# Kernel optimization log

Hardware: AMD Instinct MI355X
Metric: run time of the kernel (lower is better)

## Reference

```python
import jax, jax.numpy as jnp
import numpy as np
from jax import lax

INP_MODES = (4, 8, 8, 4)
OUT_MODES = (4, 8, 8, 4)
RANKS = (1, 8, 8, 8, 1)  # mat_ranks
WINDOW = (3, 3)


def setup_inputs() -> dict:
    key = jax.random.key(0)
    ks = jax.random.split(key, 7)
    d = {}
    d["x"] = jax.random.normal(ks[0], (16, 32, 32, 1024), jnp.float32)
    # conv filter: [kh, kw, 1, r0]
    d["filters"] = jax.random.normal(ks[1], (WINDOW[0], WINDOW[1], 1, RANKS[0]), jnp.float32) * (1.0 / 3.0)
    # TT cores: core_i has shape [m_i * r_{i+1}, r_i * n_i]
    for i in range(4):
        shp = (OUT_MODES[i] * RANKS[i + 1], RANKS[i] * INP_MODES[i])
        d[f"core{i}"] = jax.random.normal(ks[2 + i], shp, jnp.float32) * (1.0 / np.sqrt(shp[1]).astype(np.float32))
    d["bias"] = jnp.zeros((int(np.prod(OUT_MODES)),), jnp.float32)
    return d


def tt_conv(x, filters, cores, bias):
    B, H, W, C = x.shape  # C == prod(INP_MODES)
    r0 = filters.shape[3]
    # depthwise-style: every channel of every batch item becomes its own 1-channel map
    tmp = x.transpose(0, 3, 1, 2).reshape(B * C, H, W, 1)
    tmp = lax.conv_general_dilated(tmp, filters, window_strides=(1, 1), padding="SAME",
                                   dimension_numbers=("NHWC", "HWIO", "NHWC"))
    h, w = tmp.shape[1], tmp.shape[2]
    # [B, C, h, w, r0] -> [r0, C, B, h, w]
    tmp = tmp.reshape(B, C, h, w, r0).transpose(4, 1, 0, 2, 3)
    # chained TT-core contractions (fixed small loop over num_dim)
    for i in range(len(cores)):
        tmp = tmp.reshape(RANKS[i] * INP_MODES[i], -1)
        tmp = cores[i] @ tmp                      # [m_i * r_{i+1}, rest]
        tmp = tmp.reshape(OUT_MODES[i], -1).T     # move m_i to the back
    M = int(np.prod(OUT_MODES))
    out = tmp.reshape(-1, h, w, M) + bias
    return jax.nn.relu(out)


def reference(x, filters, core0, core1, core2, core3, bias):
    return tt_conv(x, filters, [core0, core1, core2, core3], bias)
```

## Files before the change

### kernel.cpp

```cpp
#include <hip/hip_runtime.h>
#include <hip/hip_bf16.h>
#include <stdint.h>

typedef __attribute__((ext_vector_type(8))) short short8;
typedef __attribute__((ext_vector_type(4))) float f32x4;

__device__ inline unsigned short f2bf(float f) {
  union { float f; unsigned u; } v; v.f = f;
  unsigned r = v.u + 0x7fffu + ((v.u >> 16) & 1u);
  return (unsigned short)(r >> 16);
}

__global__ __launch_bounds__(256) void tt_build_T(
    const float* __restrict__ c0, const float* __restrict__ c1,
    const float* __restrict__ c2, const float* __restrict__ c3,
    unsigned short* __restrict__ Tb) {
  __shared__ float L[8192];
  __shared__ float R[8192];
  int t = threadIdx.x;
  for (int i = t; i < 8192; i += 256) {
    int n1 = i & 7, n0 = (i >> 3) & 3, r2 = (i >> 5) & 7, m1 = (i >> 8) & 7, m0 = i >> 11;
    float s = 0.f;
#pragma unroll
    for (int r1 = 0; r1 < 8; ++r1)
      s += c0[(m0 * 8 + r1) * 4 + n0] * c1[(m1 * 8 + r2) * 64 + r1 * 8 + n1];
    L[i] = s;
  }
  for (int i = t; i < 8192; i += 256) {
    int n3 = i & 3, n2 = (i >> 2) & 7, m3 = (i >> 5) & 3, m2 = (i >> 7) & 7, r2 = i >> 10;
    float s = 0.f;
#pragma unroll
    for (int r3 = 0; r3 < 8; ++r3)
      s += c2[(m2 * 8 + r3) * 64 + r2 * 8 + n2] * c3[m3 * 32 + r3 * 4 + n3];
    R[i] = s;
  }
  __syncthreads();
  int base = blockIdx.x * 4096;
  for (int j = 0; j < 16; ++j) {
    int lin = j * 256 + t;
    int g = base + lin;
    int m = g >> 10, n = g & 1023;
    int m0 = m >> 8, m1 = (m >> 5) & 7, m2 = (m >> 2) & 7, m3 = m & 3;
    int n0 = n >> 8, n1 = (n >> 5) & 7, n2 = (n >> 2) & 7, n3 = n & 3;
    float s = 0.f;
#pragma unroll
    for (int r2 = 0; r2 < 8; ++r2)
      s += L[(((m0 * 8 + m1) * 8 + r2) * 4 + n0) * 8 + n1] *
           R[(((r2 * 8 + m2) * 4 + m3) * 8 + n2) * 4 + n3];
    Tb[(size_t)m * 1024 + n] = f2bf(s);
  }
}

__global__ __launch_bounds__(256) void tt_conv3x3_lds(
    const float* __restrict__ x, const float* __restrict__ filt,
    unsigned short* __restrict__ D) {
  __shared__ float xs[10][32][32];
  int bid = blockIdx.x;
  int cg = bid & 31, strip = (bid >> 5) & 3, b = bid >> 7;
  int h0 = strip * 8;
  int tid = threadIdx.x;
  float4 z4; z4.x = z4.y = z4.z = z4.w = 0.f;
#pragma unroll
  for (int i = 0; i < 10; ++i) {
    int j = tid + 256 * i;
    int row = j >> 8, w = (j >> 3) & 31, c4 = j & 7;
    int gh = h0 - 1 + row;
    float4 v = z4;
    if ((unsigned)gh < 32u)
      v = *reinterpret_cast<const float4*>(x + ((size_t)((b * 32 + gh) * 32 + w)) * 1024 + cg * 32 + c4 * 4);
    *reinterpret_cast<float4*>(&xs[row][w][c4 * 4]) = v;
  }
  float F[9];
#pragma unroll
  for (int i = 0; i < 9; ++i) F[i] = filt[i];
  __syncthreads();

  int c4 = tid & 7, w = tid >> 3;
#define LD3(r, d0, d1, d2) { \
    d1 = *reinterpret_cast<const float4*>(&xs[r][w][c4 * 4]); \
    d0 = (w > 0)  ? *reinterpret_cast<const float4*>(&xs[r][w - 1][c4 * 4]) : z4; \
    d2 = (w < 31) ? *reinterpret_cast<const float4*>(&xs[r][w + 1][c4 * 4]) : z4; }
#define ACC4(a, f, v) { a.x += (f) * v.x; a.y += (f) * v.y; a.z += (f) * v.z; a.w += (f) * v.w; }
  float4 a00, a01, a02, a10, a11, a12, a20, a21, a22;
  LD3(0, a00, a01, a02);
  LD3(1, a10, a11, a12);
#pragma unroll
  for (int h = 0; h < 8; ++h) {
    LD3(h + 2, a20, a21, a22);
    float4 s = z4;
    ACC4(s, F[0], a00); ACC4(s, F[1], a01); ACC4(s, F[2], a02);
    ACC4(s, F[3], a10); ACC4(s, F[4], a11); ACC4(s, F[5], a12);
    ACC4(s, F[6], a20); ACC4(s, F[7], a21); ACC4(s, F[8], a22);
    ushort4 o;
    o.x = f2bf(s.x); o.y = f2bf(s.y); o.z = f2bf(s.z); o.w = f2bf(s.w);
    *reinterpret_cast<ushort4*>(&D[((size_t)(b * 1024 + (h0 + h) * 32 + w)) * 1024 + cg * 32 + c4 * 4]) = o;
    a00 = a10; a01 = a11; a02 = a12;
    a10 = a20; a11 = a21; a12 = a22;
  }
#undef LD3
#undef ACC4
}

__device__ inline void stage16(const unsigned short* g, unsigned short* l) {
  __builtin_amdgcn_global_load_lds(
      (const __attribute__((address_space(1))) void*)g,
      (__attribute__((address_space(3))) void*)l, 16, 0, 0);
}

__global__ __launch_bounds__(512, 2) void tt_gemm_w1(
    const unsigned short* __restrict__ A,
    const unsigned short* __restrict__ Bt,
    const float* __restrict__ bias,
    float* __restrict__ C) {
  __shared__ unsigned short lds[3][2][8192];
  const int tid = threadIdx.x;
  const int lane = tid & 63, wave = tid >> 6;
  const int wr = wave >> 2, wc = wave & 3;
  const int lr = lane & 15, kc = lane >> 4;

  int lin = blockIdx.x + blockIdx.y * 64;
  int Lg = ((lin & 7) << 5) | (lin >> 3);
  int brow = (Lg & 63) * 256;
  int bcol = (Lg >> 6) * 256;

  int rowq0, cq0, rowq1, cq1;
  { int q = tid;       int li = q >> 3, sp = q & 7, sl = sp ^ (li & 7); rowq0 = 2 * li + (sl >> 2); cq0 = sl & 3; }
  { int q = tid + 512; int li = q >> 3, sp = q & 7, sl = sp ^ (li & 7); rowq1 = 2 * li + (sl >> 2); cq1 = sl & 3; }
  const unsigned short* srcA0 = A + (size_t)(brow + rowq0) * 1024 + cq0 * 8;
  const unsigned short* srcA1 = A + (size_t)(brow + rowq1) * 1024 + cq1 * 8;
  const unsigned short* srcB0 = Bt + (size_t)(bcol + rowq0) * 1024 + cq0 * 8;
  const unsigned short* srcB1 = Bt + (size_t)(bcol + rowq1) * 1024 + cq1 * 8;
  const int l0 = tid * 8, l1 = (tid + 512) * 8;

  int offA[8], offB[4];
#pragma unroll
  for (int m = 0; m < 8; ++m) {
    int row = wr * 128 + m * 16 + lr;
    int li = row >> 1, sl = (row & 1) * 4 + kc;
    offA[m] = (li * 8 + (sl ^ (li & 7))) * 8;
  }
#pragma unroll
  for (int n = 0; n < 4; ++n) {
    int row = wc * 64 + n * 16 + lr;
    int li = row >> 1, sl = (row & 1) * 4 + kc;
    offB[n] = (li * 8 + (sl ^ (li & 7))) * 8;
  }

  f32x4 acc[8][4] = {};

#define STAGE(S, T) { \
    stage16(srcA0 + (T) * 32, &lds[S][0][l0]); \
    stage16(srcA1 + (T) * 32, &lds[S][0][l1]); \
    stage16(srcB0 + (T) * 32, &lds[S][1][l0]); \
    stage16(srcB1 + (T) * 32, &lds[S][1][l1]); }

#define KTILE(RB, SB, T2, VMS) { \
    if ((T2) >= 0) STAGE(SB, T2); \
    asm volatile("s_waitcnt vmcnt(" VMS ")" ::: "memory"); \
    __builtin_amdgcn_s_barrier(); \
    short8 af[8], bfr[4]; \
    _Pragma("unroll") for (int m = 0; m < 8; ++m) \
      af[m] = *reinterpret_cast<const short8*>(&lds[RB][0][offA[m]]); \
    _Pragma("unroll") for (int n = 0; n < 4; ++n) \
      bfr[n] = *reinterpret_cast<const short8*>(&lds[RB][1][offB[n]]); \
    _Pragma("unroll") for (int m = 0; m < 8; ++m) \
      _Pragma("unroll") for (int n = 0; n < 4; ++n) \
        acc[m][n] = __builtin_amdgcn_mfma_f32_16x16x32_bf16(bfr[n], af[m], acc[m][n], 0, 0, 0); \
    __builtin_amdgcn_s_barrier(); \
    __builtin_amdgcn_sched_barrier(0); }

  STAGE(0, 0);
  STAGE(1, 1);

  for (int t = 0; t < 30; t += 3) {
    KTILE(0, 2, t + 2, "8")
    KTILE(1, 0, t + 3, "8")
    KTILE(2, 1, t + 4, "8")
  }
  KTILE(0, 0, -1, "4")
  KTILE(1, 1, -1, "0")

#undef KTILE
#undef STAGE

#pragma unroll
  for (int n = 0; n < 4; ++n) {
    int col = bcol + wc * 64 + n * 16 + kc * 4;
    float4 bv = *reinterpret_cast<const float4*>(&bias[col]);
#pragma unroll
    for (int m = 0; m < 8; ++m) {
      int row = brow + wr * 128 + m * 16 + lr;
      f32x4 v = acc[m][n];
      float4 o;
      o.x = v[0] + bv.x; o.y = v[1] + bv.y; o.z = v[2] + bv.z; o.w = v[3] + bv.w;
      o.x = o.x > 0.f ? o.x : 0.f;
      o.y = o.y > 0.f ? o.y : 0.f;
      o.z = o.z > 0.f ? o.z : 0.f;
      o.w = o.w > 0.f ? o.w : 0.f;
      *reinterpret_cast<float4*>(&C[(size_t)row * 1024 + col]) = o;
    }
  }
}

extern "C" void kernel_launch(void* const* d_in, const int* in_sizes, int n_in,
                              void* d_out, int out_size, void* d_ws, size_t ws_size,
                              hipStream_t stream) {
  const float* x = (const float*)d_in[0];
  const float* filt = (const float*)d_in[1];
  const float* c0 = (const float*)d_in[2];
  const float* c1 = (const float*)d_in[3];
  const float* c2 = (const float*)d_in[4];
  const float* c3 = (const float*)d_in[5];
  const float* bias = (const float*)d_in[6];
  float* out = (float*)d_out;

  unsigned short* Tb = (unsigned short*)d_ws;
  unsigned short* D = Tb + (size_t)1024 * 1024;

  tt_build_T<<<256, 256, 0, stream>>>(c0, c1, c2, c3, Tb);
  tt_conv3x3_lds<<<2048, 256, 0, stream>>>(x, filt, D);
  dim3 grid(64, 4);
  tt_gemm_w1<<<grid, 512, 0, stream>>>(D, Tb, bias, out);
}
```

Measured before the change: 80.68 us.

## Fuse 3x3 conv into GEMM mainloop, computing bf16 A tiles in LDS

```diff
diff --git a/kernel.cpp b/kernel.cpp
--- a/kernel.cpp
+++ b/kernel.cpp
@@ -3,6 +3,7 @@
 #include <stdint.h>
 
 typedef __attribute__((ext_vector_type(8))) short short8;
+typedef __attribute__((ext_vector_type(8))) unsigned short u16x8;
 typedef __attribute__((ext_vector_type(4))) float f32x4;
 
 __device__ inline unsigned short f2bf(float f) {
@@ -51,136 +52,154 @@
   }
 }
 
-__global__ __launch_bounds__(256) void tt_conv3x3_lds(
-    const float* __restrict__ x, const float* __restrict__ filt,
-    unsigned short* __restrict__ D) {
-  __shared__ float xs[10][32][32];
-  int bid = blockIdx.x;
-  int cg = bid & 31, strip = (bid >> 5) & 3, b = bid >> 7;
-  int h0 = strip * 8;
-  int tid = threadIdx.x;
-  float4 z4; z4.x = z4.y = z4.z = z4.w = 0.f;
-#pragma unroll
-  for (int i = 0; i < 10; ++i) {
-    int j = tid + 256 * i;
-    int row = j >> 8, w = (j >> 3) & 31, c4 = j & 7;
-    int gh = h0 - 1 + row;
-    float4 v = z4;
-    if ((unsigned)gh < 32u)
-      v = *reinterpret_cast<const float4*>(x + ((size_t)((b * 32 + gh) * 32 + w)) * 1024 + cg * 32 + c4 * 4);
-    *reinterpret_cast<float4*>(&xs[row][w][c4 * 4]) = v;
-  }
-  float F[9];
-#pragma unroll
-  for (int i = 0; i < 9; ++i) F[i] = filt[i];
-  __syncthreads();
-
-  int c4 = tid & 7, w = tid >> 3;
-#define LD3(r, d0, d1, d2) { \
-    d1 = *reinterpret_cast<const float4*>(&xs[r][w][c4 * 4]); \
-    d0 = (w > 0)  ? *reinterpret_cast<const float4*>(&xs[r][w - 1][c4 * 4]) : z4; \
-    d2 = (w < 31) ? *reinterpret_cast<const float4*>(&xs[r][w + 1][c4 * 4]) : z4; }
-#define ACC4(a, f, v) { a.x += (f) * v.x; a.y += (f) * v.y; a.z += (f) * v.z; a.w += (f) * v.w; }
-  float4 a00, a01, a02, a10, a11, a12, a20, a21, a22;
-  LD3(0, a00, a01, a02);
-  LD3(1, a10, a11, a12);
-#pragma unroll
-  for (int h = 0; h < 8; ++h) {
-    LD3(h + 2, a20, a21, a22);
-    float4 s = z4;
-    ACC4(s, F[0], a00); ACC4(s, F[1], a01); ACC4(s, F[2], a02);
-    ACC4(s, F[3], a10); ACC4(s, F[4], a11); ACC4(s, F[5], a12);
-    ACC4(s, F[6], a20); ACC4(s, F[7], a21); ACC4(s, F[8], a22);
-    ushort4 o;
-    o.x = f2bf(s.x); o.y = f2bf(s.y); o.z = f2bf(s.z); o.w = f2bf(s.w);
-    *reinterpret_cast<ushort4*>(&D[((size_t)(b * 1024 + (h0 + h) * 32 + w)) * 1024 + cg * 32 + c4 * 4]) = o;
-    a00 = a10; a01 = a11; a02 = a12;
-    a10 = a20; a11 = a21; a12 = a22;
-  }
-#undef LD3
-#undef ACC4
-}
-
-__device__ inline void stage16(const unsigned short* g, unsigned short* l) {
+__device__ inline void stage16(const void* g, void* l) {
   __builtin_amdgcn_global_load_lds(
       (const __attribute__((address_space(1))) void*)g,
       (__attribute__((address_space(3))) void*)l, 16, 0, 0);
 }
 
-__global__ __launch_bounds__(512, 2) void tt_gemm_w1(
-    const unsigned short* __restrict__ A,
-    const unsigned short* __restrict__ Bt,
-    const float* __restrict__ bias,
-    float* __restrict__ C) {
-  __shared__ unsigned short lds[3][2][8192];
+#define XB0 0
+#define XB1 40960
+#define AB  81920
+#define BB0 98304
+#define BB1 114688
+
+__global__ __launch_bounds__(512, 2) void tt_fused(
+    const float* __restrict__ x, const float* __restrict__ filt,
+    const unsigned short* __restrict__ Bt, const float* __restrict__ bias,
+    const float* __restrict__ zp, float* __restrict__ C) {
+  __shared__ __align__(16) char lds[131072];
   const int tid = threadIdx.x;
   const int lane = tid & 63, wave = tid >> 6;
   const int wr = wave >> 2, wc = wave & 3;
   const int lr = lane & 15, kc = lane >> 4;
 
-  int lin = blockIdx.x + blockIdx.y * 64;
-  int Lg = ((lin & 7) << 5) | (lin >> 3);
-  int brow = (Lg & 63) * 256;
-  int bcol = (Lg >> 6) * 256;
-
-  int rowq0, cq0, rowq1, cq1;
-  { int q = tid;       int li = q >> 3, sp = q & 7, sl = sp ^ (li & 7); rowq0 = 2 * li + (sl >> 2); cq0 = sl & 3; }
-  { int q = tid + 512; int li = q >> 3, sp = q & 7, sl = sp ^ (li & 7); rowq1 = 2 * li + (sl >> 2); cq1 = sl & 3; }
-  const unsigned short* srcA0 = A + (size_t)(brow + rowq0) * 1024 + cq0 * 8;
-  const unsigned short* srcA1 = A + (size_t)(brow + rowq1) * 1024 + cq1 * 8;
-  const unsigned short* srcB0 = Bt + (size_t)(bcol + rowq0) * 1024 + cq0 * 8;
-  const unsigned short* srcB1 = Bt + (size_t)(bcol + rowq1) * 1024 + cq1 * 8;
-  const int l0 = tid * 8, l1 = (tid + 512) * 8;
+  int bid = blockIdx.x;
+  int lin = (bid & 7) * 32 + (bid >> 3);
+  int np = lin >> 6, mt = lin & 63;
+  int b = mt >> 2, h0 = (mt & 3) * 8;
+  int brow = mt * 256, bcol = np * 256;
+
+  const float* xsrc[5];
+  int xstep[5], xdst[5];
+#pragma unroll
+  for (int i = 0; i < 5; ++i) {
+    int q = tid + 512 * i;
+    int r = q >> 8, w = (q >> 3) & 31;
+    int c4 = (q & 7) ^ ((w & 3) << 1);
+    int gh = h0 - 1 + r;
+    bool ok = (unsigned)gh < 32u;
+    xsrc[i] = ok ? x + (((size_t)(b * 32 + gh) * 32 + w) << 10) + c4 * 4
+                 : zp + ((q & 2047) << 2);
+    xstep[i] = ok ? 32 : 0;
+    xdst[i] = q * 16;
+  }
+  const unsigned short* bsrc[2];
+  int bdst[2];
+#pragma unroll
+  for (int j = 0; j < 2; ++j) {
+    int q = tid + 512 * j;
+    int li = q >> 3, sl = (q & 7) ^ (li & 7);
+    int row = 2 * li + (sl >> 2), ck = sl & 3;
+    bsrc[j] = Bt + (size_t)(bcol + row) * 1024 + ck * 8;
+    bdst[j] = q * 16;
+  }
+
+  const int cg = tid & 3, cw = (tid >> 2) & 31, hp = tid >> 7;
+  const int lr0 = 2 * hp;
+  int wo0, wo1;
+  {
+    int pp = lr0 * 32 + cw;
+    int li = pp >> 1, sl = (pp & 1) * 4 + cg;
+    wo0 = AB + li * 128 + (sl ^ (li & 7)) * 16;
+    pp += 32;
+    li = pp >> 1; sl = (pp & 1) * 4 + cg;
+    wo1 = AB + li * 128 + (sl ^ (li & 7)) * 16;
+  }
+  float F[9];
+#pragma unroll
+  for (int i = 0; i < 9; ++i) F[i] = filt[i];
 
   int offA[8], offB[4];
 #pragma unroll
   for (int m = 0; m < 8; ++m) {
     int row = wr * 128 + m * 16 + lr;
     int li = row >> 1, sl = (row & 1) * 4 + kc;
-    offA[m] = (li * 8 + (sl ^ (li & 7))) * 8;
+    offA[m] = AB + li * 128 + (sl ^ (li & 7)) * 16;
   }
 #pragma unroll
   for (int n = 0; n < 4; ++n) {
     int row = wc * 64 + n * 16 + lr;
     int li = row >> 1, sl = (row & 1) * 4 + kc;
-    offB[n] = (li * 8 + (sl ^ (li & 7))) * 8;
+    offB[n] = li * 128 + (sl ^ (li & 7)) * 16;
   }
 
   f32x4 acc[8][4] = {};
-
-#define STAGE(S, T) { \
-    stage16(srcA0 + (T) * 32, &lds[S][0][l0]); \
-    stage16(srcA1 + (T) * 32, &lds[S][0][l1]); \
-    stage16(srcB0 + (T) * 32, &lds[S][1][l0]); \
-    stage16(srcB1 + (T) * 32, &lds[S][1][l1]); }
-
-#define KTILE(RB, SB, T2, VMS) { \
-    if ((T2) >= 0) STAGE(SB, T2); \
-    asm volatile("s_waitcnt vmcnt(" VMS ")" ::: "memory"); \
-    __builtin_amdgcn_s_barrier(); \
+  const float4 z4 = {0.f, 0.f, 0.f, 0.f};
+
+#define STAGE(XOFF, BOFF, T) { \
+    _Pragma("unroll") for (int i = 0; i < 5; ++i) \
+      stage16(xsrc[i] + (size_t)(T) * xstep[i], lds + (XOFF) + xdst[i]); \
+    _Pragma("unroll") for (int j = 0; j < 2; ++j) \
+      stage16(bsrc[j] + (T) * 32, lds + (BOFF) + bdst[j]); }
+
+#define CONV(XOFF) { \
+    float4 s0a = z4, s0b = z4, s1a = z4, s1b = z4; \
+    _Pragma("unroll") for (int rr = 0; rr < 4; ++rr) { \
+      _Pragma("unroll") for (int dw = 0; dw < 3; ++dw) { \
+        int wq = cw + dw - 1; \
+        float4 va = z4, vb = z4; \
+        if ((unsigned)wq < 32u) { \
+          const char* p = lds + (XOFF) + (lr0 + rr) * 4096 + wq * 128 + \
+                          (((2 * cg) ^ ((wq & 3) << 1)) * 16); \
+          va = *reinterpret_cast<const float4*>(p); \
+          vb = *reinterpret_cast<const float4*>(p + 16); \
+        } \
+        if (rr < 3) { float f = F[rr * 3 + dw]; \
+          s0a.x += f * va.x; s0a.y += f * va.y; s0a.z += f * va.z; s0a.w += f * va.w; \
+          s0b.x += f * vb.x; s0b.y += f * vb.y; s0b.z += f * vb.z; s0b.w += f * vb.w; } \
+        if (rr > 0) { float f = F[(rr - 1) * 3 + dw]; \
+          s1a.x += f * va.x; s1a.y += f * va.y; s1a.z += f * va.z; s1a.w += f * va.w; \
+          s1b.x += f * vb.x; s1b.y += f * vb.y; s1b.z += f * vb.z; s1b.w += f * vb.w; } \
+      } \
+    } \
+    u16x8 o; \
+    o[0] = f2bf(s0a.x); o[1] = f2bf(s0a.y); o[2] = f2bf(s0a.z); o[3] = f2bf(s0a.w); \
+    o[4] = f2bf(s0b.x); o[5] = f2bf(s0b.y); o[6] = f2bf(s0b.z); o[7] = f2bf(s0b.w); \
+    *reinterpret_cast<u16x8*>(lds + wo0) = o; \
+    o[0] = f2bf(s1a.x); o[1] = f2bf(s1a.y); o[2] = f2bf(s1a.z); o[3] = f2bf(s1a.w); \
+    o[4] = f2bf(s1b.x); o[5] = f2bf(s1b.y); o[6] = f2bf(s1b.z); o[7] = f2bf(s1b.w); \
+    *reinterpret_cast<u16x8*>(lds + wo1) = o; }
+
+#define MFMA_PH(BOFF) { \
     short8 af[8], bfr[4]; \
     _Pragma("unroll") for (int m = 0; m < 8; ++m) \
-      af[m] = *reinterpret_cast<const short8*>(&lds[RB][0][offA[m]]); \
+      af[m] = *reinterpret_cast<const short8*>(lds + offA[m]); \
     _Pragma("unroll") for (int n = 0; n < 4; ++n) \
-      bfr[n] = *reinterpret_cast<const short8*>(&lds[RB][1][offB[n]]); \
+      bfr[n] = *reinterpret_cast<const short8*>(lds + (BOFF) + offB[n]); \
     _Pragma("unroll") for (int m = 0; m < 8; ++m) \
       _Pragma("unroll") for (int n = 0; n < 4; ++n) \
-        acc[m][n] = __builtin_amdgcn_mfma_f32_16x16x32_bf16(bfr[n], af[m], acc[m][n], 0, 0, 0); \
+        acc[m][n] = __builtin_amdgcn_mfma_f32_16x16x32_bf16(bfr[n], af[m], acc[m][n], 0, 0, 0); }
+
+#define TILE(T, XR, BR, XS, BS) { \
+    asm volatile("s_waitcnt vmcnt(0)" ::: "memory"); \
     __builtin_amdgcn_s_barrier(); \
-    __builtin_amdgcn_sched_barrier(0); }
-
-  STAGE(0, 0);
-  STAGE(1, 1);
-
-  for (int t = 0; t < 30; t += 3) {
-    KTILE(0, 2, t + 2, "8")
-    KTILE(1, 0, t + 3, "8")
-    KTILE(2, 1, t + 4, "8")
-  }
-  KTILE(0, 0, -1, "4")
-  KTILE(1, 1, -1, "0")
-
-#undef KTILE
+    asm volatile("" ::: "memory"); \
+    if ((T) + 1 < 32) STAGE(XS, BS, (T) + 1); \
+    CONV(XR); \
+    asm volatile("s_waitcnt lgkmcnt(0)" ::: "memory"); \
+    __builtin_amdgcn_s_barrier(); \
+    MFMA_PH(BR); }
+
+  STAGE(XB0, BB0, 0);
+  for (int t = 0; t < 32; t += 2) {
+    TILE(t, XB0, BB0, XB1, BB1)
+    TILE(t + 1, XB1, BB1, XB0, BB0)
+  }
+
+#undef TILE
+#undef MFMA_PH
+#undef CONV
 #undef STAGE
 
 #pragma unroll
@@ -215,10 +234,9 @@
   float* out = (float*)d_out;
 
   unsigned short* Tb = (unsigned short*)d_ws;
-  unsigned short* D = Tb + (size_t)1024 * 1024;
-
+  float* zp = (float*)((char*)d_ws + (2u << 20));
+
+  hipMemsetAsync(zp, 0, 65536, stream);
   tt_build_T<<<256, 256, 0, stream>>>(c0, c1, c2, c3, Tb);
-  tt_conv3x3_lds<<<2048, 256, 0, stream>>>(x, filt, D);
-  dim3 grid(64, 4);
-  tt_gemm_w1<<<grid, 512, 0, stream>>>(D, Tb, bias, out);
-}
+  tt_fused<<<256, 512, 0, stream>>>(x, filt, Tb, bias, zp, out);
+}
```

Result: slower. 221.1 us (+174.0%).

## Restructure GEMM mainloop into eight-phase pipeline with split A/B staging and setprio

Applied to the files above, without the earlier changes.

```diff
diff --git a/kernel.cpp b/kernel.cpp
--- a/kernel.cpp
+++ b/kernel.cpp
@@ -107,12 +107,13 @@
       (__attribute__((address_space(3))) void*)l, 16, 0, 0);
 }
 
-__global__ __launch_bounds__(512, 2) void tt_gemm_w1(
+__global__ __launch_bounds__(512, 2) void tt_gemm_8t(
     const unsigned short* __restrict__ A,
     const unsigned short* __restrict__ Bt,
     const float* __restrict__ bias,
     float* __restrict__ C) {
-  __shared__ unsigned short lds[3][2][8192];
+  __shared__ __align__(16) unsigned short Ah[2][2][8192];
+  __shared__ __align__(16) unsigned short Bh[2][2][8192];
   const int tid = threadIdx.x;
   const int lane = tid & 63, wave = tid >> 6;
   const int wr = wave >> 2, wc = wave & 3;
@@ -123,14 +124,14 @@
   int brow = (Lg & 63) * 256;
   int bcol = (Lg >> 6) * 256;
 
-  int rowq0, cq0, rowq1, cq1;
-  { int q = tid;       int li = q >> 3, sp = q & 7, sl = sp ^ (li & 7); rowq0 = 2 * li + (sl >> 2); cq0 = sl & 3; }
-  { int q = tid + 512; int li = q >> 3, sp = q & 7, sl = sp ^ (li & 7); rowq1 = 2 * li + (sl >> 2); cq1 = sl & 3; }
-  const unsigned short* srcA0 = A + (size_t)(brow + rowq0) * 1024 + cq0 * 8;
-  const unsigned short* srcA1 = A + (size_t)(brow + rowq1) * 1024 + cq1 * 8;
-  const unsigned short* srcB0 = Bt + (size_t)(bcol + rowq0) * 1024 + cq0 * 8;
-  const unsigned short* srcB1 = Bt + (size_t)(bcol + rowq1) * 1024 + cq1 * 8;
-  const int l0 = tid * 8, l1 = (tid + 512) * 8;
+  int row0, k0, row1, k1;
+  { int q = tid;       int li = q >> 3, c = (q & 7) ^ (li & 7); row0 = 2 * li + (c >> 2); k0 = (c & 3) * 8; }
+  { int q = tid + 512; int li = q >> 3, c = (q & 7) ^ (li & 7); row1 = 2 * li + (c >> 2); k1 = (c & 3) * 8; }
+  const unsigned short* pa0 = A + (size_t)(brow + row0) * 1024 + k0;
+  const unsigned short* pa1 = A + (size_t)(brow + row1) * 1024 + k1;
+  const unsigned short* pb0 = Bt + (size_t)(bcol + row0) * 1024 + k0;
+  const unsigned short* pb1 = Bt + (size_t)(bcol + row1) * 1024 + k1;
+  const int la0 = tid * 8, la1 = (tid + 512) * 8;
 
   int offA[8], offB[4];
 #pragma unroll
@@ -147,41 +148,71 @@
   }
 
   f32x4 acc[8][4] = {};
-
-#define STAGE(S, T) { \
-    stage16(srcA0 + (T) * 32, &lds[S][0][l0]); \
-    stage16(srcA1 + (T) * 32, &lds[S][0][l1]); \
-    stage16(srcB0 + (T) * 32, &lds[S][1][l0]); \
-    stage16(srcB1 + (T) * 32, &lds[S][1][l1]); }
-
-#define KTILE(RB, SB, T2, VMS) { \
-    if ((T2) >= 0) STAGE(SB, T2); \
-    asm volatile("s_waitcnt vmcnt(" VMS ")" ::: "memory"); \
+  short8 bfr[4];
+
+#define ST_A(D, KH, KT) do { \
+    stage16(pa0 + (KT) * 64 + (KH) * 32, &Ah[D][KH][la0]); \
+    stage16(pa1 + (KT) * 64 + (KH) * 32, &Ah[D][KH][la1]); } while (0)
+#define ST_B(D, KH, KT) do { \
+    stage16(pb0 + (KT) * 64 + (KH) * 32, &Bh[D][KH][la0]); \
+    stage16(pb1 + (KT) * 64 + (KH) * 32, &Bh[D][KH][la1]); } while (0)
+#define VM8 asm volatile("s_waitcnt vmcnt(8)" ::: "memory")
+#define VM4 asm volatile("s_waitcnt vmcnt(4)" ::: "memory")
+#define VM0 asm volatile("s_waitcnt vmcnt(0)" ::: "memory")
+#define NOPV (void)0
+
+#define PH(D, KK, MH, LOADB, STG, TV) { \
+    if (LOADB) { \
+      _Pragma("unroll") for (int n = 0; n < 4; ++n) \
+        bfr[n] = *reinterpret_cast<const short8*>(&Bh[D][KK][offB[n]]); \
+    } \
+    short8 af[4]; \
+    _Pragma("unroll") for (int m = 0; m < 4; ++m) \
+      af[m] = *reinterpret_cast<const short8*>(&Ah[D][KK][offA[(MH) * 4 + m]]); \
+    STG; \
     __builtin_amdgcn_s_barrier(); \
-    short8 af[8], bfr[4]; \
-    _Pragma("unroll") for (int m = 0; m < 8; ++m) \
-      af[m] = *reinterpret_cast<const short8*>(&lds[RB][0][offA[m]]); \
-    _Pragma("unroll") for (int n = 0; n < 4; ++n) \
-      bfr[n] = *reinterpret_cast<const short8*>(&lds[RB][1][offB[n]]); \
-    _Pragma("unroll") for (int m = 0; m < 8; ++m) \
+    asm volatile("s_waitcnt lgkmcnt(0)" ::: "memory"); \
+    __builtin_amdgcn_s_setprio(1); \
+    _Pragma("unroll") for (int m = 0; m < 4; ++m) \
       _Pragma("unroll") for (int n = 0; n < 4; ++n) \
-        acc[m][n] = __builtin_amdgcn_mfma_f32_16x16x32_bf16(bfr[n], af[m], acc[m][n], 0, 0, 0); \
-    __builtin_amdgcn_s_barrier(); \
-    __builtin_amdgcn_sched_barrier(0); }
-
-  STAGE(0, 0);
-  STAGE(1, 1);
-
-  for (int t = 0; t < 30; t += 3) {
-    KTILE(0, 2, t + 2, "8")
-    KTILE(1, 0, t + 3, "8")
-    KTILE(2, 1, t + 4, "8")
-  }
-  KTILE(0, 0, -1, "4")
-  KTILE(1, 1, -1, "0")
-
-#undef KTILE
-#undef STAGE
+        acc[(MH) * 4 + m][n] = __builtin_amdgcn_mfma_f32_16x16x32_bf16(bfr[n], af[m], acc[(MH) * 4 + m][n], 0, 0, 0); \
+    __builtin_amdgcn_s_setprio(0); \
+    TV; \
+    __builtin_amdgcn_s_barrier(); }
+
+  ST_A(0, 0, 0); ST_B(0, 0, 0);
+  ST_A(0, 1, 0); ST_B(0, 1, 0);
+  ST_A(1, 0, 1); ST_B(1, 0, 1);
+  VM8;
+  __builtin_amdgcn_s_barrier();
+
+  for (int i = 0; i < 7; ++i) {
+    int t = 2 * i;
+    PH(0, 0, 0, 1, ST_A(1, 1, t + 1), NOPV)
+    PH(0, 0, 1, 0, ST_B(1, 1, t + 1), VM8)
+    PH(0, 1, 0, 1, ST_A(0, 0, t + 2), NOPV)
+    PH(0, 1, 1, 0, ST_B(0, 0, t + 2), VM8)
+    PH(1, 0, 0, 1, ST_A(0, 1, t + 2), NOPV)
+    PH(1, 0, 1, 0, ST_B(0, 1, t + 2), VM8)
+    PH(1, 1, 0, 1, ST_A(1, 0, t + 3), NOPV)
+    PH(1, 1, 1, 0, ST_B(1, 0, t + 3), VM8)
+  }
+  PH(0, 0, 0, 1, ST_A(1, 1, 15), NOPV)
+  PH(0, 0, 1, 0, ST_B(1, 1, 15), VM8)
+  PH(0, 1, 0, 1, NOPV, NOPV)
+  PH(0, 1, 1, 0, NOPV, VM4)
+  PH(1, 0, 0, 1, NOPV, NOPV)
+  PH(1, 0, 1, 0, NOPV, VM0)
+  PH(1, 1, 0, 1, NOPV, NOPV)
+  PH(1, 1, 1, 0, NOPV, NOPV)
+
+#undef PH
+#undef ST_A
+#undef ST_B
+#undef VM8
+#undef VM4
+#undef VM0
+#undef NOPV
 
 #pragma unroll
   for (int n = 0; n < 4; ++n) {
@@ -220,5 +251,5 @@
   tt_build_T<<<256, 256, 0, stream>>>(c0, c1, c2, c3, Tb);
   tt_conv3x3_lds<<<2048, 256, 0, stream>>>(x, filt, D);
   dim3 grid(64, 4);
-  tt_gemm_w1<<<grid, 512, 0, stream>>>(D, Tb, bias, out);
-}
+  tt_gemm_8t<<<grid, 512, 0, stream>>>(D, Tb, bias, out);
+}
```

After: 85.38 us. +5.8%, slower.

## Merge prep kernels and register-double-buffer GEMM with 4-stage LDS ring

Applied to the files above, without the earlier changes.

```diff
diff --git a/kernel.cpp b/kernel.cpp
--- a/kernel.cpp
+++ b/kernel.cpp
@@ -10,55 +10,59 @@
   unsigned r = v.u + 0x7fffu + ((v.u >> 16) & 1u);
   return (unsigned short)(r >> 16);
 }
-
-__global__ __launch_bounds__(256) void tt_build_T(
+__device__ inline float bf2f(unsigned short u) {
+  union { unsigned u; float f; } v; v.u = ((unsigned)u) << 16; return v.f;
+}
+
+__global__ __launch_bounds__(256) void tt_prep(
+    const float* __restrict__ x, const float* __restrict__ filt,
     const float* __restrict__ c0, const float* __restrict__ c1,
     const float* __restrict__ c2, const float* __restrict__ c3,
-    unsigned short* __restrict__ Tb) {
-  __shared__ float L[8192];
-  __shared__ float R[8192];
-  int t = threadIdx.x;
-  for (int i = t; i < 8192; i += 256) {
-    int n1 = i & 7, n0 = (i >> 3) & 3, r2 = (i >> 5) & 7, m1 = (i >> 8) & 7, m0 = i >> 11;
-    float s = 0.f;
-#pragma unroll
-    for (int r1 = 0; r1 < 8; ++r1)
-      s += c0[(m0 * 8 + r1) * 4 + n0] * c1[(m1 * 8 + r2) * 64 + r1 * 8 + n1];
-    L[i] = s;
-  }
-  for (int i = t; i < 8192; i += 256) {
-    int n3 = i & 3, n2 = (i >> 2) & 7, m3 = (i >> 5) & 3, m2 = (i >> 7) & 7, r2 = i >> 10;
-    float s = 0.f;
-#pragma unroll
-    for (int r3 = 0; r3 < 8; ++r3)
-      s += c2[(m2 * 8 + r3) * 64 + r2 * 8 + n2] * c3[m3 * 32 + r3 * 4 + n3];
-    R[i] = s;
-  }
-  __syncthreads();
-  int base = blockIdx.x * 4096;
-  for (int j = 0; j < 16; ++j) {
-    int lin = j * 256 + t;
-    int g = base + lin;
-    int m = g >> 10, n = g & 1023;
-    int m0 = m >> 8, m1 = (m >> 5) & 7, m2 = (m >> 2) & 7, m3 = m & 3;
-    int n0 = n >> 8, n1 = (n >> 5) & 7, n2 = (n >> 2) & 7, n3 = n & 3;
-    float s = 0.f;
-#pragma unroll
-    for (int r2 = 0; r2 < 8; ++r2)
-      s += L[(((m0 * 8 + m1) * 8 + r2) * 4 + n0) * 8 + n1] *
-           R[(((r2 * 8 + m2) * 4 + m3) * 8 + n2) * 4 + n3];
-    Tb[(size_t)m * 1024 + n] = f2bf(s);
-  }
-}
-
-__global__ __launch_bounds__(256) void tt_conv3x3_lds(
-    const float* __restrict__ x, const float* __restrict__ filt,
-    unsigned short* __restrict__ D) {
-  __shared__ float xs[10][32][32];
-  int bid = blockIdx.x;
-  int cg = bid & 31, strip = (bid >> 5) & 3, b = bid >> 7;
+    unsigned short* __restrict__ Tb, unsigned short* __restrict__ D) {
+  __shared__ __align__(16) char smem[40960];
+  const int tid = threadIdx.x;
+  const int bid = blockIdx.x;
+
+  if (bid < 256) {
+    unsigned short* Lb = (unsigned short*)smem;
+    unsigned short* Rb = (unsigned short*)(smem + 16384);
+    for (int i = tid; i < 8192; i += 256) {
+      int n1 = i & 7, n0 = (i >> 3) & 3, r2 = (i >> 5) & 7, m1 = (i >> 8) & 7, m0 = i >> 11;
+      float s = 0.f;
+#pragma unroll
+      for (int r1 = 0; r1 < 8; ++r1)
+        s += c0[(m0 * 8 + r1) * 4 + n0] * c1[(m1 * 8 + r2) * 64 + r1 * 8 + n1];
+      Lb[i] = f2bf(s);
+    }
+    for (int i = tid; i < 8192; i += 256) {
+      int n3 = i & 3, n2 = (i >> 2) & 7, m3 = (i >> 5) & 3, m2 = (i >> 7) & 7, r2 = i >> 10;
+      float s = 0.f;
+#pragma unroll
+      for (int r3 = 0; r3 < 8; ++r3)
+        s += c2[(m2 * 8 + r3) * 64 + r2 * 8 + n2] * c3[m3 * 32 + r3 * 4 + n3];
+      Rb[i] = f2bf(s);
+    }
+    __syncthreads();
+    int base = bid * 4096;
+    for (int j = 0; j < 16; ++j) {
+      int g = base + j * 256 + tid;
+      int m = g >> 10, n = g & 1023;
+      int m0 = m >> 8, m1 = (m >> 5) & 7, m2 = (m >> 2) & 7, m3 = m & 3;
+      int n0 = n >> 8, n1 = (n >> 5) & 7, n2 = (n >> 2) & 7, n3 = n & 3;
+      float s = 0.f;
+#pragma unroll
+      for (int r2 = 0; r2 < 8; ++r2)
+        s += bf2f(Lb[(((m0 * 8 + m1) * 8 + r2) * 4 + n0) * 8 + n1]) *
+             bf2f(Rb[(((r2 * 8 + m2) * 4 + m3) * 8 + n2) * 4 + n3]);
+      Tb[(size_t)m * 1024 + n] = f2bf(s);
+    }
+    return;
+  }
+
+  float (*xs)[32][32] = (float(*)[32][32])smem;
+  int cb = bid - 256;
+  int cg = cb & 31, strip = (cb >> 5) & 3, b = cb >> 7;
   int h0 = strip * 8;
-  int tid = threadIdx.x;
   float4 z4; z4.x = z4.y = z4.z = z4.w = 0.f;
 #pragma unroll
   for (int i = 0; i < 10; ++i) {
@@ -107,12 +111,12 @@
       (__attribute__((address_space(3))) void*)l, 16, 0, 0);
 }
 
-__global__ __launch_bounds__(512, 2) void tt_gemm_w1(
+__global__ __launch_bounds__(512, 2) void tt_gemm_rb(
     const unsigned short* __restrict__ A,
     const unsigned short* __restrict__ Bt,
     const float* __restrict__ bias,
     float* __restrict__ C) {
-  __shared__ unsigned short lds[3][2][8192];
+  __shared__ unsigned short lds[4][16384];
   const int tid = threadIdx.x;
   const int lane = tid & 63, wave = tid >> 6;
   const int wr = wave >> 2, wc = wave & 3;
@@ -123,14 +127,14 @@
   int brow = (Lg & 63) * 256;
   int bcol = (Lg >> 6) * 256;
 
-  int rowq0, cq0, rowq1, cq1;
-  { int q = tid;       int li = q >> 3, sp = q & 7, sl = sp ^ (li & 7); rowq0 = 2 * li + (sl >> 2); cq0 = sl & 3; }
-  { int q = tid + 512; int li = q >> 3, sp = q & 7, sl = sp ^ (li & 7); rowq1 = 2 * li + (sl >> 2); cq1 = sl & 3; }
-  const unsigned short* srcA0 = A + (size_t)(brow + rowq0) * 1024 + cq0 * 8;
-  const unsigned short* srcA1 = A + (size_t)(brow + rowq1) * 1024 + cq1 * 8;
-  const unsigned short* srcB0 = Bt + (size_t)(bcol + rowq0) * 1024 + cq0 * 8;
-  const unsigned short* srcB1 = Bt + (size_t)(bcol + rowq1) * 1024 + cq1 * 8;
-  const int l0 = tid * 8, l1 = (tid + 512) * 8;
+  int row0, k0, row1, k1;
+  { int q = tid;       int li = q >> 3, c = (q & 7) ^ (li & 7); row0 = 2 * li + (c >> 2); k0 = (c & 3) * 8; }
+  { int q = tid + 512; int li = q >> 3, c = (q & 7) ^ (li & 7); row1 = 2 * li + (c >> 2); k1 = (c & 3) * 8; }
+  const unsigned short* pa0 = A + (size_t)(brow + row0) * 1024 + k0;
+  const unsigned short* pa1 = A + (size_t)(brow + row1) * 1024 + k1;
+  const unsigned short* pb0 = Bt + (size_t)(bcol + row0) * 1024 + k0;
+  const unsigned short* pb1 = Bt + (size_t)(bcol + row1) * 1024 + k1;
+  const int la0 = tid * 8, la1 = (tid + 512) * 8;
 
   int offA[8], offB[4];
 #pragma unroll
@@ -143,44 +147,55 @@
   for (int n = 0; n < 4; ++n) {
     int row = wc * 64 + n * 16 + lr;
     int li = row >> 1, sl = (row & 1) * 4 + kc;
-    offB[n] = (li * 8 + (sl ^ (li & 7))) * 8;
+    offB[n] = 8192 + (li * 8 + (sl ^ (li & 7))) * 8;
   }
 
   f32x4 acc[8][4] = {};
+  short8 a0[8], b0[4], a1[8], b1[4];
 
 #define STAGE(S, T) { \
-    stage16(srcA0 + (T) * 32, &lds[S][0][l0]); \
-    stage16(srcA1 + (T) * 32, &lds[S][0][l1]); \
-    stage16(srcB0 + (T) * 32, &lds[S][1][l0]); \
-    stage16(srcB1 + (T) * 32, &lds[S][1][l1]); }
-
-#define KTILE(RB, SB, T2, VMS) { \
-    if ((T2) >= 0) STAGE(SB, T2); \
+    stage16(pa0 + (T) * 32, &lds[S][la0]); \
+    stage16(pa1 + (T) * 32, &lds[S][la1]); \
+    stage16(pb0 + (T) * 32, &lds[S][8192 + la0]); \
+    stage16(pb1 + (T) * 32, &lds[S][8192 + la1]); }
+
+#define READF(AF, BF, S) { \
+    _Pragma("unroll") for (int m = 0; m < 8; ++m) \
+      AF[m] = *reinterpret_cast<const short8*>(&lds[S][offA[m]]); \
+    _Pragma("unroll") for (int n = 0; n < 4; ++n) \
+      BF[n] = *reinterpret_cast<const short8*>(&lds[S][offB[n]]); }
+
+#define MFMAS(AF, BF) { \
+    _Pragma("unroll") for (int m = 0; m < 8; ++m) \
+      _Pragma("unroll") for (int n = 0; n < 4; ++n) \
+        acc[m][n] = __builtin_amdgcn_mfma_f32_16x16x32_bf16(BF[n], AF[m], acc[m][n], 0, 0, 0); }
+
+#define ITER(T, AFc, BFc, AFn, BFn, DOSTAGE, VMS) { \
+    asm volatile("s_waitcnt lgkmcnt(12)" ::: "memory"); \
     asm volatile("s_waitcnt vmcnt(" VMS ")" ::: "memory"); \
     __builtin_amdgcn_s_barrier(); \
-    short8 af[8], bfr[4]; \
-    _Pragma("unroll") for (int m = 0; m < 8; ++m) \
-      af[m] = *reinterpret_cast<const short8*>(&lds[RB][0][offA[m]]); \
-    _Pragma("unroll") for (int n = 0; n < 4; ++n) \
-      bfr[n] = *reinterpret_cast<const short8*>(&lds[RB][1][offB[n]]); \
-    _Pragma("unroll") for (int m = 0; m < 8; ++m) \
-      _Pragma("unroll") for (int n = 0; n < 4; ++n) \
-        acc[m][n] = __builtin_amdgcn_mfma_f32_16x16x32_bf16(bfr[n], af[m], acc[m][n], 0, 0, 0); \
-    __builtin_amdgcn_s_barrier(); \
-    __builtin_amdgcn_sched_barrier(0); }
-
-  STAGE(0, 0);
-  STAGE(1, 1);
-
-  for (int t = 0; t < 30; t += 3) {
-    KTILE(0, 2, t + 2, "8")
-    KTILE(1, 0, t + 3, "8")
-    KTILE(2, 1, t + 4, "8")
-  }
-  KTILE(0, 0, -1, "4")
-  KTILE(1, 1, -1, "0")
-
-#undef KTILE
+    if (DOSTAGE) STAGE(((T) + 3) & 3, (T) + 3); \
+    READF(AFn, BFn, ((T) + 1) & 3); \
+    MFMAS(AFc, BFc); }
+
+  STAGE(0, 0); STAGE(1, 1); STAGE(2, 2);
+  asm volatile("s_waitcnt vmcnt(8)" ::: "memory");
+  __builtin_amdgcn_s_barrier();
+  READF(a0, b0, 0);
+
+  for (int tp = 0; tp < 14; ++tp) {
+    int t = 2 * tp;
+    ITER(t,     a0, b0, a1, b1, 1, "4")
+    ITER(t + 1, a1, b1, a0, b0, 1, "4")
+  }
+  ITER(28, a0, b0, a1, b1, 1, "4")
+  ITER(29, a1, b1, a0, b0, 0, "4")
+  ITER(30, a0, b0, a1, b1, 0, "0")
+  MFMAS(a1, b1);
+
+#undef ITER
+#undef MFMAS
+#undef READF
 #undef STAGE
 
 #pragma unroll
@@ -217,8 +232,7 @@
   unsigned short* Tb = (unsigned short*)d_ws;
   unsigned short* D = Tb + (size_t)1024 * 1024;
 
-  tt_build_T<<<256, 256, 0, stream>>>(c0, c1, c2, c3, Tb);
-  tt_conv3x3_lds<<<2048, 256, 0, stream>>>(x, filt, D);
+  tt_prep<<<2304, 256, 0, stream>>>(x, filt, c0, c1, c2, c3, Tb, D);
   dim3 grid(64, 4);
-  tt_gemm_w1<<<grid, 512, 0, stream>>>(D, Tb, bias, out);
-}
+  tt_gemm_rb<<<grid, 512, 0, stream>>>(D, Tb, bias, out);
+}
```

Result: faster. 72.32 us (-10.4%).
